# Kernel tuning notes

Measured on AMD Instinct MI355X. Metric: run time of the kernel, lower is better.

Reference implementation:

```python
import jax, jax.numpy as jnp
import numpy as np

H = 16
LN_EPS = 1e-5


def setup_inputs() -> dict:
    key = jax.random.key(0)
    ks = jax.random.split(key, 8)
    B, N, D = 2, 2048, 1024
    s = D ** -0.5
    return {
        "q_s": jax.random.normal(ks[0], (B, N, D), jnp.float32),
        "pos_emb": jax.random.normal(ks[1], (B, N, D), jnp.float32),
        "Wq": jax.random.normal(ks[2], (D, D), jnp.float32) * s,
        "Wk": jax.random.normal(ks[3], (D, D), jnp.float32) * s,
        "Wv": jax.random.normal(ks[4], (D, D), jnp.float32) * s,
        "Wo": jax.random.normal(ks[5], (D, D), jnp.float32) * s,
        "bo": jnp.zeros((D,), jnp.float32),
        "ln_g": jnp.ones((D,), jnp.float32),
        "ln_b": jnp.zeros((D,), jnp.float32),
    }


def _split_heads(t):
    b, n, d = t.shape
    return t.reshape(b, n, H, d // H).transpose(0, 2, 1, 3)  # b h n d


def reference(q_s, pos_emb, Wq, Wk, Wv, Wo, bo, ln_g, ln_b):
    # self-attention: k_s = v_s = q_s
    q = _split_heads(q_s @ Wq)
    k = _split_heads(q_s @ Wk)
    v = _split_heads(q_s @ Wv)
    p = _split_heads(pos_emb)
    scale = q.shape[-1] ** -0.5
    # content-content + content-position attention logits: [b,h,i,j]
    att = (jnp.einsum('bhid,bhjd->bhij', q, k) + jnp.einsum('bhid,bhjd->bhij', q, p)) * scale
    att = jax.nn.softmax(att, axis=-1)
    o = jnp.einsum('bhij,bhjd->bhid', att, v)
    b, h, n, d = o.shape
    o = o.transpose(0, 2, 1, 3).reshape(b, n, h * d)
    o = o @ Wo + bo  # out_layer (dropout rate 0 -> identity)
    x = o + q_s  # residual
    mu = jnp.mean(x, axis=-1, keepdims=True)
    var = jnp.var(x, axis=-1, keepdims=True)
    return (x - mu) * jax.lax.rsqrt(var + LN_EPS) * ln_g + ln_b
```

## Files before the change

### kernel.cpp

```cpp
#include <hip/hip_runtime.h>
#include <hip/hip_bf16.h>
#include <stdint.h>

typedef unsigned short u16;
typedef unsigned int u32;
typedef short s16x8 __attribute__((ext_vector_type(8)));
typedef short s16x4 __attribute__((ext_vector_type(4)));
typedef float f32x4 __attribute__((ext_vector_type(4)));

#define MFMA(a, b, c) __builtin_amdgcn_mfma_f32_16x16x32_bf16((a), (b), (c), 0, 0, 0)

__device__ __forceinline__ float bf2f(u16 h) {
  u32 u = ((u32)h) << 16;
  float f;
  __builtin_memcpy(&f, &u, 4);
  return f;
}

__device__ __forceinline__ u16 f2bf_rte(float f) {
  __hip_bfloat16 h = __float2bfloat16(f);
  u16 u;
  __builtin_memcpy(&u, &h, 2);
  return u;
}

__device__ __forceinline__ void gload16(const u16* g, u16* l) {
  __builtin_amdgcn_global_load_lds((const __attribute__((address_space(1))) u32*)g,
                                   (__attribute__((address_space(3))) u32*)l, 16, 0, 0);
}

__global__ __launch_bounds__(256) void k_prep(const float* __restrict__ q_s,
                                              const float* __restrict__ pos,
                                              const float* __restrict__ W0,
                                              const float* __restrict__ W1,
                                              const float* __restrict__ W2,
                                              const float* __restrict__ W3,
                                              u16* __restrict__ Xbf,
                                              u16* __restrict__ Pp,
                                              u16* __restrict__ WT) {
  __shared__ u16 tile[64][65];
  const int b = blockIdx.x;
  const int t = threadIdx.x;
  if (b < 2048) {
    const int i = b * 256 + t;
    const f32x4* p = (const f32x4*)(q_s + (size_t)i * 8);
    f32x4 a = p[0], bb = p[1];
    s16x8 o;
    for (int k = 0; k < 4; ++k) o[k] = (short)f2bf_rte(a[k]);
    for (int k = 0; k < 4; ++k) o[4 + k] = (short)f2bf_rte(bb[k]);
    *(s16x8*)(Xbf + (size_t)i * 8) = o;
  } else if (b < 3072) {
    const int pb = b - 2048;
    const int bh = pb >> 5, bx = pb & 31;
    const int bq = bh >> 4, h = bh & 15;
    const int n = bx * 64 + (t >> 2);
    const int d0 = (t & 3) * 16;
    const float* src = &pos[((size_t)(bq * 2048 + n)) * 1024 + h * 64 + d0];
    u16* dst = &Pp[((size_t)bh * 2048 + n) * 64 + d0];
    f32x4 a = *(const f32x4*)src;
    f32x4 bq4 = *(const f32x4*)(src + 4);
    f32x4 c = *(const f32x4*)(src + 8);
    f32x4 dq = *(const f32x4*)(src + 12);
    s16x8 o0, o1;
    for (int i = 0; i < 4; ++i) {
      o0[i] = (short)f2bf_rte(a[i]);
      o0[4 + i] = (short)f2bf_rte(bq4[i]);
      o1[i] = (short)f2bf_rte(c[i]);
      o1[4 + i] = (short)f2bf_rte(dq[i]);
    }
    *(s16x8*)dst = o0;
    *(s16x8*)(dst + 8) = o1;
  } else {
    const int wb = b - 3072;
    const int z = wb >> 8, r2 = wb & 255;
    const int bx = r2 & 15, by = r2 >> 4;
    const float* in = (z == 0) ? W0 : (z == 1) ? W1 : (z == 2) ? W2 : W3;
    u16* o = WT + (size_t)z * 1024 * 1024;
    const int tx = t & 63, ty = t >> 6;
    const int r0 = by * 64, c0 = bx * 64;
    for (int rr = 0; rr < 16; ++rr) {
      int row = rr * 4 + ty;
      tile[row][tx] = f2bf_rte(in[(size_t)(r0 + row) * 1024 + c0 + tx]);
    }
    __syncthreads();
    for (int rr = 0; rr < 16; ++rr) {
      int row = rr * 4 + ty;
      o[(size_t)(c0 + row) * 1024 + r0 + tx] = tile[tx][row];
    }
  }
}

__global__ __launch_bounds__(256) void k_transpose_v(const u16* __restrict__ V,
                                                     u16* __restrict__ Vt) {
  __shared__ u16 tile[64][65];
  const int t = threadIdx.x, tx = t & 63, ty = t >> 6;
  const int j0 = blockIdx.x * 64;
  const int bh = blockIdx.y;
  const u16* src = V + (size_t)bh * 2048 * 64;
  u16* dst = Vt + (size_t)bh * 64 * 2048;
  for (int rr = 0; rr < 16; ++rr) {
    int row = rr * 4 + ty;
    tile[row][tx] = src[(size_t)(j0 + row) * 64 + tx];
  }
  __syncthreads();
  for (int rr = 0; rr < 16; ++rr) {
    int d = rr * 4 + ty;
    dst[(size_t)d * 2048 + j0 + tx] = tile[tx][d];
  }
}

__global__ __launch_bounds__(256) void k_qkv_gemm(const u16* __restrict__ X,
                                                  const u16* __restrict__ WT,
                                                  const u16* __restrict__ Pp,
                                                  u16* __restrict__ Qh,
                                                  u16* __restrict__ Kh,
                                                  u16* __restrict__ Vh) {
  __shared__ u16 As[3][4096];
  __shared__ u16 Bs[3][4096];
  const int t = threadIdx.x;
  const int lane = t & 63, wid = t >> 6;
  const int wr = wid >> 1, wc = wid & 1;
  const int g = lane >> 4, lr = lane & 15;
  const int lin = blockIdx.y * 24 + blockIdx.x;
  const int swz = (lin & 7) * 96 + (lin >> 3);
  const int m0 = (swz / 24) * 128, n0 = (swz % 24) * 128;

  const int srcRow = t >> 2;
  const int srcKsw = ((t & 3) * 8) ^ (((t >> 3) & 3) << 3);
  const u16* aSrc = &X[(size_t)(m0 + srcRow) * 1024 + srcKsw];
  const u16* bSrc = &WT[(size_t)(n0 + srcRow) * 1024 + srcKsw];

  const int csw = (g * 8) ^ (((lr >> 1) & 3) << 3);

  f32x4 acc[4][4] = {};

#define QKV_STAGE(buf, k0)                                   \
  {                                                          \
    gload16(aSrc + (k0), &As[buf][wid * 512]);               \
    gload16(aSrc + 65536 + (k0), &As[buf][wid * 512 + 2048]);\
    gload16(bSrc + (k0), &Bs[buf][wid * 512]);               \
    gload16(bSrc + 65536 + (k0), &Bs[buf][wid * 512 + 2048]);\
  }

  QKV_STAGE(0, 0);
  QKV_STAGE(1, 32);
  QKV_STAGE(2, 64);
  for (int k = 0; k < 32; ++k) {
    if (k < 30) {
      asm volatile("s_waitcnt vmcnt(8)" ::: "memory");
    } else if (k == 30) {
      asm volatile("s_waitcnt vmcnt(4)" ::: "memory");
    } else {
      asm volatile("s_waitcnt vmcnt(0)" ::: "memory");
    }
    __builtin_amdgcn_sched_barrier(0);
    __builtin_amdgcn_s_barrier();
    const int cur = k % 3;
    s16x8 a[4], b[4];
#pragma unroll
    for (int mi = 0; mi < 4; ++mi)
      a[mi] = *(const s16x8*)&As[cur][(wr * 64 + mi * 16 + lr) * 32 + csw];
#pragma unroll
    for (int nj = 0; nj < 4; ++nj)
      b[nj] = *(const s16x8*)&Bs[cur][(wc * 64 + nj * 16 + lr) * 32 + csw];
#pragma unroll
    for (int mi = 0; mi < 4; ++mi)
#pragma unroll
      for (int nj = 0; nj < 4; ++nj)
        acc[mi][nj] = MFMA(a[mi], b[nj], acc[mi][nj]);
    __builtin_amdgcn_s_barrier();
    if (k < 29) QKV_STAGE(cur, (k + 3) * 32);
  }
#undef QKV_STAGE

  const float QSCALE = 0.125f * 1.44269504f;
  for (int mi = 0; mi < 4; ++mi) {
    for (int nj = 0; nj < 4; ++nj) {
      const int n_g = n0 + wc * 64 + nj * 16 + lr;
      const int buf = n_g >> 10;
      const int col = n_g & 1023;
      const int h = col >> 6, d = col & 63;
      u16* dst = (buf == 0) ? Qh : ((buf == 1) ? Kh : Vh);
      for (int r = 0; r < 4; ++r) {
        const int row = m0 + wr * 64 + mi * 16 + g * 4 + r;
        const int b = row >> 11, n = row & 2047;
        const size_t off = (size_t)((b * 16 + h) * 2048 + n) * 64 + d;
        float v = acc[mi][nj][r];
        if (buf == 1) v += bf2f(Pp[off]);
        if (buf == 0) v *= QSCALE;
        dst[off] = f2bf_rte(v);
      }
    }
  }
}

__global__ __launch_bounds__(512, 4) void k_attn(const u16* __restrict__ Qh,
                                                 const u16* __restrict__ Kh,
                                                 const u16* __restrict__ Vt,
                                                 u16* __restrict__ Oh) {
  const int t = threadIdx.x, lane = t & 63, wid = t >> 6;
  const int g = lane >> 4, lr = lane & 15;
  const int hid = blockIdx.x;
  const int lid = (hid & 7) * 64 + (hid >> 3);
  const int bh = lid >> 4, itile = lid & 15;
  const int i0 = itile * 128 + wid * 16;

  __shared__ char Ks[4][8192];
  __shared__ char Vs[4][8192];

  const u16* Qp = Qh + (size_t)bh * 2048 * 64;
  const u16* Kp = Kh + (size_t)bh * 2048 * 64;
  const u16* Vp = Vt + (size_t)bh * 64 * 2048;

  s16x8 aq[2];
  aq[0] = *(const s16x8*)&Qp[(size_t)(i0 + lr) * 64 + g * 8];
  aq[1] = *(const s16x8*)&Qp[(size_t)(i0 + lr) * 64 + 32 + g * 8];

  f32x4 oa[4] = {};
  float ms = -1e30f, ls = 0.f;

  const int srow = t >> 3;
  const int sch = (t & 7) * 16;
  const int schS = sch ^ ((srow & 7) << 4);
  const u16* kB = &Kp[(size_t)srow * 64 + (schS >> 1)];
  const u16* vB = &Vp[(size_t)srow * 2048 + (schS >> 1)];

#define ATTN_STAGE(p)                                                \
  {                                                                  \
    gload16(kB + (size_t)(p) * 4096, (u16*)Ks[(p) & 3] + wid * 512); \
    gload16(vB + (size_t)(p) * 64, (u16*)Vs[(p) & 3] + wid * 512);   \
  }

#define ATTN_BODY(BUF)                                                         \
  {                                                                            \
    const char* Kc = Ks[BUF];                                                  \
    const char* Vc = Vs[BUF];                                                  \
    f32x4 s[4] = {};                                                           \
    _Pragma("unroll") for (int jf = 0; jf < 4; ++jf) {                         \
      const int row = jf * 16 + lr;                                            \
      const int bw = (row & 7) << 4;                                           \
      s16x8 bk0 = *(const s16x8*)(Kc + ((row * 128 + g * 16) ^ bw));           \
      s16x8 bk1 = *(const s16x8*)(Kc + ((row * 128 + 64 + g * 16) ^ bw));      \
      s[jf] = MFMA(bk0, aq[0], s[jf]);                                         \
      s[jf] = MFMA(bk1, aq[1], s[jf]);                                         \
    }                                                                          \
    float mj[4];                                                               \
    _Pragma("unroll") for (int jf = 0; jf < 4; ++jf)                           \
        mj[jf] = fmaxf(fmaxf(s[jf][0], s[jf][1]), fmaxf(s[jf][2], s[jf][3]));  \
    float tl = fmaxf(fmaxf(mj[0], mj[1]), fmaxf(mj[2], mj[3]));                \
    if (!__all(tl <= ms + 8.f)) {                                              \
      float tm = fmaxf(tl, __shfl_xor(tl, 16, 64));                            \
      tm = fmaxf(tm, __shfl_xor(tm, 32, 64));                                  \
      float mn = fmaxf(ms, tm);                                                \
      float al = __builtin_amdgcn_exp2f(ms - mn);                              \
      ls *= al;                                                                \
      ms = mn;                                                                 \
      _Pragma("unroll") for (int r = 0; r < 4; ++r) {                          \
        float ab = __shfl(al, g * 4 + r, 64);                                  \
        _Pragma("unroll") for (int df = 0; df < 4; ++df) oa[df][r] *= ab;      \
      }                                                                        \
    }                                                                          \
    float pj[4];                                                               \
    _Pragma("unroll") for (int jf = 0; jf < 4; ++jf) {                         \
      _Pragma("unroll") for (int r = 0; r < 4; ++r)                            \
          s[jf][r] = __builtin_amdgcn_exp2f(s[jf][r] - ms);                    \
      pj[jf] = (s[jf][0] + s[jf][1]) + (s[jf][2] + s[jf][3]);                  \
    }                                                                          \
    ls += (pj[0] + pj[1]) + (pj[2] + pj[3]);                                   \
    u32 pk[4][2];                                                              \
    _Pragma("unroll") for (int jf = 0; jf < 4; ++jf) {                         \
      asm("v_cvt_pk_bf16_f32 %0, %1, %2"                                       \
          : "=v"(pk[jf][0]) : "v"(s[jf][0]), "v"(s[jf][1]));                   \
      asm("v_cvt_pk_bf16_f32 %0, %1, %2"                                       \
          : "=v"(pk[jf][1]) : "v"(s[jf][2]), "v"(s[jf][3]));                   \
    }                                                                          \
    s16x8 pa[2];                                                               \
    _Pragma("unroll") for (int c = 0; c < 2; ++c) {                            \
      u32 w_[4];                                                               \
      _Pragma("unroll") for (int wl = 0; wl < 2; ++wl) {                       \
        u32 A = pk[2 * c][wl], B = pk[2 * c + 1][wl];                          \
        asm("v_permlane32_swap_b32 %0, %1" : "+v"(A), "+v"(B));                \
        asm("v_permlane16_swap_b32 %0, %1" : "+v"(A), "+v"(B));                \
        w_[wl] = A;                                                            \
        w_[2 + wl] = B;                                                        \
      }                                                                        \
      __builtin_memcpy(&pa[c], w_, 16);                                        \
    }                                                                          \
    _Pragma("unroll") for (int df = 0; df < 4; ++df) {                         \
      const int row = df * 16 + lr;                                            \
      const int bw = (row & 7) << 4;                                           \
      s16x8 bv0 = *(const s16x8*)(Vc + ((row * 128 + g * 16) ^ bw));           \
      s16x8 bv1 = *(const s16x8*)(Vc + ((row * 128 + 64 + g * 16) ^ bw));      \
      oa[df] = MFMA(pa[0], bv0, oa[df]);                                       \
      oa[df] = MFMA(pa[1], bv1, oa[df]);                                       \
    }                                                                          \
  }

  ATTN_STAGE(0);
  ATTN_STAGE(1);
  ATTN_STAGE(2);

  for (int tb = 0; tb < 7; ++tb) {
#pragma unroll
    for (int ti = 0; ti < 4; ++ti) {
      const int tt = tb * 4 + ti;
      asm volatile("s_waitcnt vmcnt(4)" ::: "memory");
      __builtin_amdgcn_sched_barrier(0);
      __builtin_amdgcn_s_barrier();
      ATTN_STAGE(tt + 3);
      ATTN_BODY(ti);
    }
  }
  {
    asm volatile("s_waitcnt vmcnt(4)" ::: "memory");
    __builtin_amdgcn_sched_barrier(0);
    __builtin_amdgcn_s_barrier();
    ATTN_STAGE(31);
    ATTN_BODY(0);
  }
  {
    asm volatile("s_waitcnt vmcnt(4)" ::: "memory");
    __builtin_amdgcn_sched_barrier(0);
    __builtin_amdgcn_s_barrier();
    ATTN_BODY(1);
  }
  {
    asm volatile("s_waitcnt vmcnt(2)" ::: "memory");
    __builtin_amdgcn_sched_barrier(0);
    __builtin_amdgcn_s_barrier();
    ATTN_BODY(2);
  }
  {
    asm volatile("s_waitcnt vmcnt(0)" ::: "memory");
    __builtin_amdgcn_sched_barrier(0);
    __builtin_amdgcn_s_barrier();
    ATTN_BODY(3);
  }
#undef ATTN_BODY
#undef ATTN_STAGE

  ls += __shfl_xor(ls, 16, 64);
  ls += __shfl_xor(ls, 32, 64);
  float lb[4];
#pragma unroll
  for (int r = 0; r < 4; ++r) lb[r] = __shfl(ls, g * 4 + r, 64);

  u16* Op = Oh + (size_t)bh * 2048 * 64;
#pragma unroll
  for (int df = 0; df < 4; ++df)
#pragma unroll
    for (int r = 0; r < 4; ++r) {
      const int row0 = i0 + g * 4 + r;
      Op[(size_t)row0 * 64 + df * 16 + lr] = f2bf_rte(oa[df][r] / lb[r]);
    }
}

__global__ __launch_bounds__(256) void k_out_gemm(const u16* __restrict__ Oh,
                                                  const u16* __restrict__ WTo,
                                                  const float* __restrict__ bo,
                                                  const u16* __restrict__ qsb,
                                                  u16* __restrict__ X) {
  __shared__ u16 As[3][4096];
  __shared__ u16 Bs[3][4096];
  const int t = threadIdx.x;
  const int lane = t & 63, wid = t >> 6;
  const int wr = wid >> 1, wc = wid & 1;
  const int g = lane >> 4, lr = lane & 15;
  const int lin = blockIdx.y * 8 + blockIdx.x;
  const int swz = (lin & 7) * 32 + (lin >> 3);
  const int m0 = (swz / 8) * 128, n0 = (swz % 8) * 128;

  const int srcRow = t >> 2;
  const int srcKsw = ((t & 3) * 8) ^ (((t >> 3) & 3) << 3);
  const int rg = m0 + srcRow, bb0 = rg >> 11, nn0 = rg & 2047;
  const int rg2 = rg + 64, bb2 = rg2 >> 11, nn2 = rg2 & 2047;
  const u16* bSrc = &WTo[(size_t)(n0 + srcRow) * 1024 + srcKsw];
  const int csw = (g * 8) ^ (((lr >> 1) & 3) << 3);

  f32x4 acc[4][4] = {};

#define OUT_STAGE(buf, k0)                                                        \
  {                                                                               \
    const int h_ = (k0) >> 6, d_ = ((k0) & 63) + srcKsw;                          \
    gload16(&Oh[((size_t)(bb0 * 16 + h_) * 2048 + nn0) * 64 + d_],                \
            &As[buf][wid * 512]);                                                 \
    gload16(&Oh[((size_t)(bb2 * 16 + h_) * 2048 + nn2) * 64 + d_],                \
            &As[buf][wid * 512 + 2048]);                                          \
    gload16(bSrc + (k0), &Bs[buf][wid * 512]);                                    \
    gload16(bSrc + 65536 + (k0), &Bs[buf][wid * 512 + 2048]);                     \
  }

  OUT_STAGE(0, 0);
  OUT_STAGE(1, 32);
  OUT_STAGE(2, 64);
  for (int k = 0; k < 32; ++k) {
    if (k < 30) {
      asm volatile("s_waitcnt vmcnt(8)" ::: "memory");
    } else if (k == 30) {
      asm volatile("s_waitcnt vmcnt(4)" ::: "memory");
    } else {
      asm volatile("s_waitcnt vmcnt(0)" ::: "memory");
    }
    __builtin_amdgcn_sched_barrier(0);
    __builtin_amdgcn_s_barrier();
    const int cur = k % 3;
    s16x8 a[4], b[4];
#pragma unroll
    for (int mi = 0; mi < 4; ++mi)
      a[mi] = *(const s16x8*)&As[cur][(wr * 64 + mi * 16 + lr) * 32 + csw];
#pragma unroll
    for (int nj = 0; nj < 4; ++nj)
      b[nj] = *(const s16x8*)&Bs[cur][(wc * 64 + nj * 16 + lr) * 32 + csw];
#pragma unroll
    for (int mi = 0; mi < 4; ++mi)
#pragma unroll
      for (int nj = 0; nj < 4; ++nj)
        acc[mi][nj] = MFMA(a[mi], b[nj], acc[mi][nj]);
    __builtin_amdgcn_s_barrier();
    if (k < 29) OUT_STAGE(cur, (k + 3) * 32);
  }
#undef OUT_STAGE

  for (int mi = 0; mi < 4; ++mi) {
    for (int nj = 0; nj < 4; ++nj) {
      const int col = n0 + wc * 64 + nj * 16 + lr;
      for (int r = 0; r < 4; ++r) {
        const int row = m0 + wr * 64 + mi * 16 + g * 4 + r;
        float v = acc[mi][nj][r] + bo[col] + bf2f(qsb[(size_t)row * 1024 + col]);
        X[(size_t)row * 1024 + col] = f2bf_rte(v);
      }
    }
  }
}

__global__ __launch_bounds__(256) void k_ln(const u16* __restrict__ X,
                                            const float* __restrict__ gg,
                                            const float* __restrict__ bb,
                                            float* __restrict__ out) {
  const int row = blockIdx.x, t = threadIdx.x;
  const int wid = t >> 6, lane = t & 63;
  const u16* xr = X + (size_t)row * 1024;
  s16x4 xv = *(const s16x4*)&xr[t * 4];
  float x[4];
  for (int i = 0; i < 4; ++i) x[i] = bf2f((u16)xv[i]);
  float s1 = (x[0] + x[1]) + (x[2] + x[3]);
  float s2 = (x[0] * x[0] + x[1] * x[1]) + (x[2] * x[2] + x[3] * x[3]);
  for (int off = 32; off > 0; off >>= 1) {
    s1 += __shfl_down(s1, off, 64);
    s2 += __shfl_down(s2, off, 64);
  }
  __shared__ float red[2][4];
  if (lane == 0) { red[0][wid] = s1; red[1][wid] = s2; }
  __syncthreads();
  s1 = red[0][0] + red[0][1] + red[0][2] + red[0][3];
  s2 = red[1][0] + red[1][1] + red[1][2] + red[1][3];
  const float mu = s1 * (1.f / 1024.f);
  const float var = s2 * (1.f / 1024.f) - mu * mu;
  const float rstd = rsqrtf(var + 1e-5f);
  f32x4 gv = *(const f32x4*)&gg[t * 4];
  f32x4 bv = *(const f32x4*)&bb[t * 4];
  f32x4 ov;
  for (int i = 0; i < 4; ++i) ov[i] = (x[i] - mu) * rstd * gv[i] + bv[i];
  *(f32x4*)&out[(size_t)row * 1024 + t * 4] = ov;
}

extern "C" void kernel_launch(void* const* d_in, const int* in_sizes, int n_in,
                              void* d_out, int out_size, void* d_ws, size_t ws_size,
                              hipStream_t stream) {
  (void)in_sizes; (void)n_in; (void)out_size; (void)ws_size;
  const float* q_s = (const float*)d_in[0];
  const float* pos = (const float*)d_in[1];
  const float* Wq = (const float*)d_in[2];
  const float* Wk = (const float*)d_in[3];
  const float* Wv = (const float*)d_in[4];
  const float* Wo = (const float*)d_in[5];
  const float* bo = (const float*)d_in[6];
  const float* lng = (const float*)d_in[7];
  const float* lnb = (const float*)d_in[8];
  float* out = (float*)d_out;

  u16* ws = (u16*)d_ws;
  const size_t MB1 = 1024 * 1024;
  u16* WT  = ws;
  u16* Xbf = ws + 4 * MB1;
  u16* Qh  = Xbf + 4 * MB1;
  u16* Kh  = Qh + 4 * MB1;
  u16* Vh  = Kh + 4 * MB1;
  u16* Vt  = Vh + 4 * MB1;
  u16* Oh  = Vt + 4 * MB1;
  u16* Pp  = Oh;
  u16* Xb  = Qh;

  dim3 blk(256);
  k_prep<<<dim3(4096), blk, 0, stream>>>(q_s, pos, Wq, Wk, Wv, Wo, Xbf, Pp, WT);
  k_qkv_gemm<<<dim3(24, 32), blk, 0, stream>>>(Xbf, WT, Pp, Qh, Kh, Vh);
  k_transpose_v<<<dim3(32, 32), blk, 0, stream>>>(Vh, Vt);
  k_attn<<<dim3(512), dim3(512), 0, stream>>>(Qh, Kh, Vt, Oh);
  k_out_gemm<<<dim3(8, 32), blk, 0, stream>>>(Oh, WT + 3 * MB1, bo, Xbf, Xb);
  k_ln<<<4096, blk, 0, stream>>>(Xb, lng, lnb, out);
}
```

Baseline: 142.6 us.

## Split attention over two key halves and merge with a combine kernel

The attention kernel now splits the key/value sequence into two halves, launching twice as many blocks. Each block writes unnormalized bf16 partial outputs plus per-row max and sum, and a new combine kernel rescales and merges the two halves in place. The K/V pipeline drops from four-stage to double-buffered shared memory, waiting on all loads each step. This is meant to raise occupancy and CU coverage at the cost of an extra launch, extra partial-output traffic, and rounding unnormalized accumulators to bf16.

```diff
diff --git a/kernel.cpp b/kernel.cpp
--- a/kernel.cpp
+++ b/kernel.cpp
@@ -197,16 +197,18 @@
 __global__ __launch_bounds__(512, 4) void k_attn(const u16* __restrict__ Qh,
                                                  const u16* __restrict__ Kh,
                                                  const u16* __restrict__ Vt,
-                                                 u16* __restrict__ Oh) {
+                                                 u16* __restrict__ P0,
+                                                 u16* __restrict__ P1,
+                                                 float* __restrict__ ML) {
   const int t = threadIdx.x, lane = t & 63, wid = t >> 6;
   const int g = lane >> 4, lr = lane & 15;
   const int hid = blockIdx.x;
-  const int lid = (hid & 7) * 64 + (hid >> 3);
-  const int bh = lid >> 4, itile = lid & 15;
+  const int lid = (hid & 7) * 128 + (hid >> 3);
+  const int bh = lid >> 5, itile = (lid >> 1) & 15, jh = lid & 1;
   const int i0 = itile * 128 + wid * 16;
 
-  __shared__ char Ks[4][8192];
-  __shared__ char Vs[4][8192];
+  __shared__ char Ks[2][8192];
+  __shared__ char Vs[2][8192];
 
   const u16* Qp = Qh + (size_t)bh * 2048 * 64;
   const u16* Kp = Kh + (size_t)bh * 2048 * 64;
@@ -222,13 +224,13 @@
   const int srow = t >> 3;
   const int sch = (t & 7) * 16;
   const int schS = sch ^ ((srow & 7) << 4);
-  const u16* kB = &Kp[(size_t)srow * 64 + (schS >> 1)];
-  const u16* vB = &Vp[(size_t)srow * 2048 + (schS >> 1)];
-
-#define ATTN_STAGE(p)                                                \
-  {                                                                  \
-    gload16(kB + (size_t)(p) * 4096, (u16*)Ks[(p) & 3] + wid * 512); \
-    gload16(vB + (size_t)(p) * 64, (u16*)Vs[(p) & 3] + wid * 512);   \
+  const u16* kB = &Kp[(size_t)(jh * 1024 + srow) * 64 + (schS >> 1)];
+  const u16* vB = &Vp[(size_t)srow * 2048 + jh * 1024 + (schS >> 1)];
+
+#define ATTN_STAGE(p, B)                                   \
+  {                                                        \
+    gload16(kB + (size_t)(p) * 4096, (u16*)Ks[B] + wid * 512); \
+    gload16(vB + (size_t)(p) * 64, (u16*)Vs[B] + wid * 512);   \
   }
 
 #define ATTN_BODY(BUF)                                                         \
@@ -296,63 +298,68 @@
     }                                                                          \
   }
 
-  ATTN_STAGE(0);
-  ATTN_STAGE(1);
-  ATTN_STAGE(2);
-
-  for (int tb = 0; tb < 7; ++tb) {
-#pragma unroll
-    for (int ti = 0; ti < 4; ++ti) {
-      const int tt = tb * 4 + ti;
-      asm volatile("s_waitcnt vmcnt(4)" ::: "memory");
+  ATTN_STAGE(0, 0);
+
+  for (int th = 0; th < 8; ++th) {
+#pragma unroll
+    for (int ti = 0; ti < 2; ++ti) {
+      const int tt = th * 2 + ti;
+      asm volatile("s_waitcnt vmcnt(0)" ::: "memory");
       __builtin_amdgcn_sched_barrier(0);
       __builtin_amdgcn_s_barrier();
-      ATTN_STAGE(tt + 3);
+      if (tt < 15) ATTN_STAGE(tt + 1, ti ^ 1);
       ATTN_BODY(ti);
     }
-  }
-  {
-    asm volatile("s_waitcnt vmcnt(4)" ::: "memory");
-    __builtin_amdgcn_sched_barrier(0);
-    __builtin_amdgcn_s_barrier();
-    ATTN_STAGE(31);
-    ATTN_BODY(0);
-  }
-  {
-    asm volatile("s_waitcnt vmcnt(4)" ::: "memory");
-    __builtin_amdgcn_sched_barrier(0);
-    __builtin_amdgcn_s_barrier();
-    ATTN_BODY(1);
-  }
-  {
-    asm volatile("s_waitcnt vmcnt(2)" ::: "memory");
-    __builtin_amdgcn_sched_barrier(0);
-    __builtin_amdgcn_s_barrier();
-    ATTN_BODY(2);
-  }
-  {
-    asm volatile("s_waitcnt vmcnt(0)" ::: "memory");
-    __builtin_amdgcn_sched_barrier(0);
-    __builtin_amdgcn_s_barrier();
-    ATTN_BODY(3);
   }
 #undef ATTN_BODY
 #undef ATTN_STAGE
 
   ls += __shfl_xor(ls, 16, 64);
   ls += __shfl_xor(ls, 32, 64);
-  float lb[4];
-#pragma unroll
-  for (int r = 0; r < 4; ++r) lb[r] = __shfl(ls, g * 4 + r, 64);
-
-  u16* Op = Oh + (size_t)bh * 2048 * 64;
+
+  if (lane < 16) {
+    const size_t ridx = (size_t)jh * 65536 + (size_t)bh * 2048 + i0 + lr;
+    ML[ridx] = ms;
+    ML[131072 + ridx] = ls;
+  }
+
+  u16* Op = (jh ? P1 : P0) + (size_t)bh * 2048 * 64;
 #pragma unroll
   for (int df = 0; df < 4; ++df)
 #pragma unroll
     for (int r = 0; r < 4; ++r) {
       const int row0 = i0 + g * 4 + r;
-      Op[(size_t)row0 * 64 + df * 16 + lr] = f2bf_rte(oa[df][r] / lb[r]);
-    }
+      Op[(size_t)row0 * 64 + df * 16 + lr] = f2bf_rte(oa[df][r]);
+    }
+}
+
+__global__ __launch_bounds__(256) void k_combine(u16* __restrict__ O,
+                                                 const u16* __restrict__ P1,
+                                                 const float* __restrict__ ML) {
+  const int t = threadIdx.x;
+  const size_t R = (size_t)blockIdx.x * 64 + (t >> 2);
+  const int d0 = (t & 3) * 16;
+  const float m0 = ML[R], m1 = ML[65536 + R];
+  const float l0 = ML[131072 + R], l1 = ML[196608 + R];
+  const float M = fmaxf(m0, m1);
+  const float s0 = __builtin_amdgcn_exp2f(m0 - M);
+  const float s1 = __builtin_amdgcn_exp2f(m1 - M);
+  const float inv = 1.f / (l0 * s0 + l1 * s1);
+  const float f0 = s0 * inv, f1 = s1 * inv;
+  u16* o = O + R * 64 + d0;
+  const u16* p = P1 + R * 64 + d0;
+  s16x8 a0 = *(const s16x8*)o;
+  s16x8 a1 = *(const s16x8*)(o + 8);
+  s16x8 b0 = *(const s16x8*)p;
+  s16x8 b1 = *(const s16x8*)(p + 8);
+  s16x8 r0, r1;
+#pragma unroll
+  for (int i = 0; i < 8; ++i) {
+    r0[i] = (short)f2bf_rte(bf2f((u16)a0[i]) * f0 + bf2f((u16)b0[i]) * f1);
+    r1[i] = (short)f2bf_rte(bf2f((u16)a1[i]) * f0 + bf2f((u16)b1[i]) * f1);
+  }
+  *(s16x8*)o = r0;
+  *(s16x8*)(o + 8) = r1;
 }
 
 __global__ __launch_bounds__(256) void k_out_gemm(const u16* __restrict__ Oh,
@@ -489,13 +496,16 @@
   u16* Vt  = Vh + 4 * MB1;
   u16* Oh  = Vt + 4 * MB1;
   u16* Pp  = Oh;
+  u16* P1  = Oh + 4 * MB1;
+  float* ML = (float*)(P1 + 4 * MB1);
   u16* Xb  = Qh;
 
   dim3 blk(256);
   k_prep<<<dim3(4096), blk, 0, stream>>>(q_s, pos, Wq, Wk, Wv, Wo, Xbf, Pp, WT);
   k_qkv_gemm<<<dim3(24, 32), blk, 0, stream>>>(Xbf, WT, Pp, Qh, Kh, Vh);
   k_transpose_v<<<dim3(32, 32), blk, 0, stream>>>(Vh, Vt);
-  k_attn<<<dim3(512), dim3(512), 0, stream>>>(Qh, Kh, Vt, Oh);
+  k_attn<<<dim3(1024), dim3(512), 0, stream>>>(Qh, Kh, Vt, Oh, P1, ML);
+  k_combine<<<dim3(1024), blk, 0, stream>>>(Oh, P1, ML);
   k_out_gemm<<<dim3(8, 32), blk, 0, stream>>>(Oh, WT + 3 * MB1, bo, Xbf, Xb);
   k_ln<<<4096, blk, 0, stream>>>(Xb, lng, lnb, out);
 }
```

After: 147.4 us. 1.03x slower.
